# Performance work log

Hardware: AMD Instinct MI355X
Metric: run time of the kernel (lower is better)

Reference implementation:

```python
import jax, jax.numpy as jnp
import numpy as np

BOHR = 0.52917721067  # Angstrom per Bohr (au.BOHR)
A_MUTUAL = 0.39       # damping_param_mutual
N_NODES = 200_000
N_EDGES = 6_400_000


def setup_inputs() -> dict:
    key = jax.random.key(0)
    k1, k2, k3, k4, k5, k6 = jax.random.split(key, 6)
    edge_src = jax.random.randint(k1, (N_EDGES,), 0, N_NODES)
    edge_dst = jax.random.randint(k2, (N_EDGES,), 0, N_NODES)
    # displacement vectors (Angstrom); distances consistent with vec
    vec = jax.random.normal(k3, (N_EDGES, 3), dtype=jnp.float32) * 2.0
    distances = jnp.linalg.norm(vec, axis=-1) + 1e-3
    # positive polarisabilities (Angstrom^3)
    polarisability = jax.random.uniform(k4, (N_NODES,), dtype=jnp.float32) * 2.0 + 0.5
    mu = jax.random.normal(k5, (N_NODES, 3), dtype=jnp.float32) * 0.1
    species = jax.random.randint(k6, (N_NODES,), 0, 10)
    return {
        'species': species,
        'edge_src': edge_src,
        'edge_dst': edge_dst,
        'distances': distances,
        'vec': vec,
        'polarisability': polarisability,
        'mu': mu,
    }


def reference(species, edge_src, edge_dst, distances, vec, polarisability, mu):
    n_nodes = polarisability.shape[0]
    rij = distances / BOHR                 # [E]
    vec_ij = vec / BOHR                    # [E,3]
    pol = polarisability / BOHR**3         # [N]
    alpha_ij = pol[edge_dst] * pol[edge_src]   # [E]
    uij = rij / alpha_ij ** (1.0 / 6.0)
    au3 = A_MUTUAL * uij**3
    e = jnp.exp(-au3)
    lam3 = 1.0 - e                         # Thole lambda_3
    lam5 = 1.0 - (1.0 + au3) * e           # Thole lambda_5
    # Thole-damped dipole interaction matvec: T_ij mu_j
    mu_dst = mu[edge_dst]                  # [E,3] gather
    inv_r3 = 1.0 / rij**3
    inv_r5 = 1.0 / rij**5
    dot = jnp.sum(vec_ij * mu_dst, axis=-1)   # [E]
    contrib = (lam3 * inv_r3)[:, None] * mu_dst \
        - (3.0 * lam5 * inv_r5 * dot)[:, None] * vec_ij  # [E,3]
    field = jax.ops.segment_sum(contrib, edge_src, num_segments=n_nodes)  # [N,3]
    # diagonal 1/alpha term of the polarisation matrix
    return mu / pol[:, None] + field
```

## Files before the change

kernel.cpp:

```cpp
#include <hip/hip_runtime.h>
#include <math.h>


#define INV_BOHR   1.8897261254578281f
#define INV_BOHR3  (INV_BOHR*INV_BOHR*INV_BOHR)
#define A_MUTUAL   0.39f
#define NB         256
#define EPB        4096
#define SCT        512
#define GAT        1024
#define MAX_NPB    1024
#define GC_STRIDE  16

typedef float f32x4 __attribute__((ext_vector_type(4)));

__global__ void pol_node_kernel(const float* __restrict__ pol_ang,
                                const float* __restrict__ mu,
                                float* __restrict__ out,
                                float* __restrict__ q, int n_nodes) {
    int i = blockIdx.x * blockDim.x + threadIdx.x;
    if (i >= n_nodes) return;
    float pol = pol_ang[i] * INV_BOHR3;
    float ip  = 1.0f / pol;
    out[3*i + 0] = mu[3*i + 0] * ip;
    out[3*i + 1] = mu[3*i + 1] * ip;
    out[3*i + 2] = mu[3*i + 2] * ip;
    q[i] = powf(pol, -1.0f / 6.0f);
}

__device__ __forceinline__ void thole_contrib(
        float rij, float vx, float vy, float vz,
        float qs, float qd, float mx, float my, float mz,
        float& cx, float& cy, float& cz) {
    float u   = rij * qs * qd;
    float au3 = A_MUTUAL * u * u * u;
    float em1  = expm1f(-au3);
    float lam3 = -em1;
    float lam5 = -(em1 + au3 * (em1 + 1.0f));
    float inv_r  = 1.0f / rij;
    float inv_r2 = inv_r * inv_r;
    float inv_r3 = inv_r2 * inv_r;
    float inv_r5 = inv_r3 * inv_r2;
    float dot = vx*mx + vy*my + vz*mz;
    float c3  = lam3 * inv_r3;
    float c5  = 3.0f * lam5 * inv_r5 * dot;
    cx = c3*mx - c5*vx;
    cy = c3*my - c5*vy;
    cz = c3*mz - c5*vz;
}

__global__ __launch_bounds__(SCT, 4)
void pol_scatter(const int*   __restrict__ src,
                 const int*   __restrict__ dst,
                 const float* __restrict__ dist,
                 const float* __restrict__ vec,
                 const float* __restrict__ q,
                 const float* __restrict__ mu,
                 f32x4*       __restrict__ records,
                 int*         __restrict__ gcursor,
                 int e0, int e1, int npb, int cap) {
    __shared__ f32x4 stage[EPB];
    __shared__ int hist[NB];
    __shared__ int lbase[NB];
    __shared__ int scan[NB];
    __shared__ int lcur[NB];
    __shared__ int gbase[NB];

    int tid = threadIdx.x;
    int eb0 = e0 + blockIdx.x * EPB;
    int eb1 = min(eb0 + EPB, e1);
    int nrec = eb1 - eb0;
    if (nrec <= 0) return;

    if (tid < NB) hist[tid] = 0;
    __syncthreads();

    int s_reg[EPB / SCT];
    #pragma unroll
    for (int j = 0; j < EPB / SCT; ++j) {
        int e = eb0 + j * SCT + tid;
        int s = (e < eb1) ? src[e] : -1;
        s_reg[j] = s;
        if (s >= 0) atomicAdd(&hist[s / npb], 1);
    }
    __syncthreads();

    if (tid < NB) scan[tid] = hist[tid];
    __syncthreads();
    for (int off = 1; off < NB; off <<= 1) {
        int v = 0;
        if (tid < NB && tid >= off) v = scan[tid - off];
        __syncthreads();
        if (tid < NB) scan[tid] += v;
        __syncthreads();
    }
    if (tid < NB) {
        int lb = scan[tid] - hist[tid];
        lbase[tid] = lb;
        lcur[tid]  = lb;
        gbase[tid] = (hist[tid] > 0) ? atomicAdd(&gcursor[tid * GC_STRIDE], hist[tid]) : 0;
    }
    __syncthreads();

    #pragma unroll
    for (int j = 0; j < EPB / SCT; ++j) {
        int s = s_reg[j];
        if (s < 0) continue;
        int e = eb0 + j * SCT + tid;
        int   d   = __builtin_nontemporal_load(&dst[e]);
        float rij = __builtin_nontemporal_load(&dist[e]) * INV_BOHR;
        float vx  = __builtin_nontemporal_load(&vec[3*e + 0]) * INV_BOHR;
        float vy  = __builtin_nontemporal_load(&vec[3*e + 1]) * INV_BOHR;
        float vz  = __builtin_nontemporal_load(&vec[3*e + 2]) * INV_BOHR;

        float cx, cy, cz;
        thole_contrib(rij, vx, vy, vz, q[s], q[d],
                      mu[3*d + 0], mu[3*d + 1], mu[3*d + 2], cx, cy, cz);

        int b = s / npb;
        int p = atomicAdd(&lcur[b], 1);
        f32x4 rec;
        rec.x = cx; rec.y = cy; rec.z = cz; rec.w = __int_as_float(s);
        stage[p] = rec;
    }
    __syncthreads();

    for (int k = tid; k < nrec; k += SCT) {
        f32x4 f = stage[k];
        int s = __float_as_int(f.w);
        int b = s / npb;
        int slot = gbase[b] + (k - lbase[b]);
        if (slot < cap)
            records[(size_t)b * cap + slot] = f;
    }
}

__global__ __launch_bounds__(GAT, 4)
void pol_gather(const f32x4* __restrict__ records,
                const int*   __restrict__ gcursor,
                float*       __restrict__ out,
                int cap, int npb, int n_nodes) {
    __shared__ float acc[3 * MAX_NPB];
    int j   = blockIdx.x;
    int tid = threadIdx.x;
    int n0  = j * npb;
    int nn  = min(npb, n_nodes - n0);
    if (nn <= 0) return;

    for (int k = tid; k < 3 * nn; k += GAT) acc[k] = 0.0f;
    __syncthreads();

    int cnt = min(gcursor[j * GC_STRIDE], cap);
    const f32x4* rec = records + (size_t)j * cap;

    int i = tid;
    for (; i + 3 * GAT < cnt; i += 4 * GAT) {
        f32x4 r0 = __builtin_nontemporal_load(&rec[i]);
        f32x4 r1 = __builtin_nontemporal_load(&rec[i + GAT]);
        f32x4 r2 = __builtin_nontemporal_load(&rec[i + 2 * GAT]);
        f32x4 r3 = __builtin_nontemporal_load(&rec[i + 3 * GAT]);
        int l0 = __float_as_int(r0.w) - n0;
        int l1 = __float_as_int(r1.w) - n0;
        int l2 = __float_as_int(r2.w) - n0;
        int l3 = __float_as_int(r3.w) - n0;
        atomicAdd(&acc[3*l0 + 0], r0.x); atomicAdd(&acc[3*l0 + 1], r0.y); atomicAdd(&acc[3*l0 + 2], r0.z);
        atomicAdd(&acc[3*l1 + 0], r1.x); atomicAdd(&acc[3*l1 + 1], r1.y); atomicAdd(&acc[3*l1 + 2], r1.z);
        atomicAdd(&acc[3*l2 + 0], r2.x); atomicAdd(&acc[3*l2 + 1], r2.y); atomicAdd(&acc[3*l2 + 2], r2.z);
        atomicAdd(&acc[3*l3 + 0], r3.x); atomicAdd(&acc[3*l3 + 1], r3.y); atomicAdd(&acc[3*l3 + 2], r3.z);
    }
    for (; i < cnt; i += GAT) {
        f32x4 r = __builtin_nontemporal_load(&rec[i]);
        int l = __float_as_int(r.w) - n0;
        atomicAdd(&acc[3*l + 0], r.x);
        atomicAdd(&acc[3*l + 1], r.y);
        atomicAdd(&acc[3*l + 2], r.z);
    }
    __syncthreads();

    float* o = out + (size_t)3 * n0;
    for (int k = tid; k < 3 * nn; k += GAT) o[k] += acc[k];
}

__global__ void pol_edge_kernel(const int*   __restrict__ src,
                                const int*   __restrict__ dst,
                                const float* __restrict__ dist,
                                const float* __restrict__ vec,
                                const float* __restrict__ q,
                                const float* __restrict__ mu,
                                float* __restrict__ out, int n_edges) {
    int e = blockIdx.x * blockDim.x + threadIdx.x;
    if (e >= n_edges) return;
    int s = src[e], d = dst[e];
    float rij = dist[e] * INV_BOHR;
    float cx, cy, cz;
    thole_contrib(rij, vec[3*e+0]*INV_BOHR, vec[3*e+1]*INV_BOHR, vec[3*e+2]*INV_BOHR,
                  q[s], q[d], mu[3*d+0], mu[3*d+1], mu[3*d+2], cx, cy, cz);
    atomicAdd(&out[3*s + 0], cx);
    atomicAdd(&out[3*s + 1], cy);
    atomicAdd(&out[3*s + 2], cz);
}

extern "C" void kernel_launch(void* const* d_in, const int* in_sizes, int n_in,
                              void* d_out, int out_size, void* d_ws, size_t ws_size,
                              hipStream_t stream) {
    const int*   edge_src = (const int*)d_in[1];
    const int*   edge_dst = (const int*)d_in[2];
    const float* dist     = (const float*)d_in[3];
    const float* vec      = (const float*)d_in[4];
    const float* pol      = (const float*)d_in[5];
    const float* mu       = (const float*)d_in[6];

    float* out   = (float*)d_out;
    int n_nodes  = in_sizes[5];
    int n_edges  = in_sizes[1];
    int npb      = (n_nodes + NB - 1) / NB;

    size_t gc_bytes = (size_t)NB * GC_STRIDE * sizeof(int);
    size_t reserve  = gc_bytes + (size_t)n_nodes * sizeof(float) + 4096;
    int    nch = -1;
    long long cap = 0;
    size_t rec_bytes = 0;
    for (int c = 1; c <= 16; c *= 2) {
        long long chunk = ((long long)n_edges + c - 1) / c;
        long long m     = (chunk + NB - 1) / NB;
        long long cp    = m + 8 * (long long)(sqrt((double)m) + 1.0) + 64;
        size_t rb = (size_t)NB * (size_t)cp * sizeof(f32x4);
        if (rb + reserve <= ws_size) { nch = c; cap = cp; rec_bytes = rb; break; }
    }

    if (nch > 0 && npb <= MAX_NPB) {
        f32x4* records = (f32x4*)d_ws;
        int*   gcursor = (int*)((char*)d_ws + rec_bytes);
        float* q       = (float*)((char*)d_ws + rec_bytes + gc_bytes);

        pol_node_kernel<<<(n_nodes + 255) / 256, 256, 0, stream>>>(pol, mu, out, q, n_nodes);

        long long chunk = ((long long)n_edges + nch - 1) / nch;
        for (int r = 0; r < nch; ++r) {
            int e0 = (int)(r * chunk);
            int e1 = (int)min((long long)n_edges, e0 + chunk);
            if (e0 >= e1) break;
            (void)hipMemsetAsync(gcursor, 0, gc_bytes, stream);
            int nblk = (e1 - e0 + EPB - 1) / EPB;
            pol_scatter<<<nblk, SCT, 0, stream>>>(edge_src, edge_dst, dist, vec, q, mu,
                                                  records, gcursor, e0, e1, npb, (int)cap);
            pol_gather<<<NB, GAT, 0, stream>>>(records, gcursor, out, (int)cap, npb, n_nodes);
        }
    } else {
        float* q = (float*)d_ws;
        pol_node_kernel<<<(n_nodes + 255) / 256, 256, 0, stream>>>(pol, mu, out, q, n_nodes);
        pol_edge_kernel<<<(n_edges + 255) / 256, 256, 0, stream>>>(edge_src, edge_dst, dist, vec,
                                                                   q, mu, out, n_edges);
    }
}
```

Measured before the change: 426.5 us.

## Pack q and mu per node, use magic-number division, halve edges per block

The node kernel now writes a packed float4 holding (mu, q) per node, so the scatter kernel fetches the destination's q and mu with one 16-byte gather instead of four scattered loads. Integer division by npb is replaced with a multiply-shift magic number. EPB is halved and launch bounds raised to 8 to increase occupancy, src loads become nontemporal, and the gather loop is unrolled to 8 outstanding loads. The packed array is four times larger than the old q array, and the smaller blocks mean more blocks and more global cursor atomics.

Result: faster. 403.8 us (-5.3%).

```diff
diff --git a/kernel.cpp b/kernel.cpp
--- a/kernel.cpp
+++ b/kernel.cpp
@@ -6,26 +6,33 @@
 #define INV_BOHR3  (INV_BOHR*INV_BOHR*INV_BOHR)
 #define A_MUTUAL   0.39f
 #define NB         256
-#define EPB        4096
+#define EPB        2048
 #define SCT        512
 #define GAT        1024
 #define MAX_NPB    1024
 #define GC_STRIDE  16
+#define MSHIFT     40
 
 typedef float f32x4 __attribute__((ext_vector_type(4)));
+
+__device__ __forceinline__ int bdiv(int s, unsigned magic) {
+    return (int)(((unsigned long long)(unsigned)s * magic) >> MSHIFT);
+}
 
 __global__ void pol_node_kernel(const float* __restrict__ pol_ang,
                                 const float* __restrict__ mu,
                                 float* __restrict__ out,
-                                float* __restrict__ q, int n_nodes) {
+                                f32x4* __restrict__ qmu, int n_nodes) {
     int i = blockIdx.x * blockDim.x + threadIdx.x;
     if (i >= n_nodes) return;
     float pol = pol_ang[i] * INV_BOHR3;
     float ip  = 1.0f / pol;
-    out[3*i + 0] = mu[3*i + 0] * ip;
-    out[3*i + 1] = mu[3*i + 1] * ip;
-    out[3*i + 2] = mu[3*i + 2] * ip;
-    q[i] = powf(pol, -1.0f / 6.0f);
+    float mx = mu[3*i + 0], my = mu[3*i + 1], mz = mu[3*i + 2];
+    out[3*i + 0] = mx * ip;
+    out[3*i + 1] = my * ip;
+    out[3*i + 2] = mz * ip;
+    f32x4 t; t.x = mx; t.y = my; t.z = mz; t.w = powf(pol, -1.0f / 6.0f);
+    qmu[i] = t;
 }
 
 __device__ __forceinline__ void thole_contrib(
@@ -49,16 +56,15 @@
     cz = c3*mz - c5*vz;
 }
 
-__global__ __launch_bounds__(SCT, 4)
+__global__ __launch_bounds__(SCT, 8)
 void pol_scatter(const int*   __restrict__ src,
                  const int*   __restrict__ dst,
                  const float* __restrict__ dist,
                  const float* __restrict__ vec,
-                 const float* __restrict__ q,
-                 const float* __restrict__ mu,
+                 const f32x4* __restrict__ qmu,
                  f32x4*       __restrict__ records,
                  int*         __restrict__ gcursor,
-                 int e0, int e1, int npb, int cap) {
+                 int e0, int e1, int npb, int cap, unsigned magic) {
     __shared__ f32x4 stage[EPB];
     __shared__ int hist[NB];
     __shared__ int lbase[NB];
@@ -79,9 +85,9 @@
     #pragma unroll
     for (int j = 0; j < EPB / SCT; ++j) {
         int e = eb0 + j * SCT + tid;
-        int s = (e < eb1) ? src[e] : -1;
+        int s = (e < eb1) ? __builtin_nontemporal_load(&src[e]) : -1;
         s_reg[j] = s;
-        if (s >= 0) atomicAdd(&hist[s / npb], 1);
+        if (s >= 0) atomicAdd(&hist[bdiv(s, magic)], 1);
     }
     __syncthreads();
 
@@ -113,11 +119,13 @@
         float vy  = __builtin_nontemporal_load(&vec[3*e + 1]) * INV_BOHR;
         float vz  = __builtin_nontemporal_load(&vec[3*e + 2]) * INV_BOHR;
 
+        f32x4 md = qmu[d];
+        float qs = qmu[s].w;
+
         float cx, cy, cz;
-        thole_contrib(rij, vx, vy, vz, q[s], q[d],
-                      mu[3*d + 0], mu[3*d + 1], mu[3*d + 2], cx, cy, cz);
-
-        int b = s / npb;
+        thole_contrib(rij, vx, vy, vz, qs, md.w, md.x, md.y, md.z, cx, cy, cz);
+
+        int b = bdiv(s, magic);
         int p = atomicAdd(&lcur[b], 1);
         f32x4 rec;
         rec.x = cx; rec.y = cy; rec.z = cz; rec.w = __int_as_float(s);
@@ -128,7 +136,7 @@
     for (int k = tid; k < nrec; k += SCT) {
         f32x4 f = stage[k];
         int s = __float_as_int(f.w);
-        int b = s / npb;
+        int b = bdiv(s, magic);
         int slot = gbase[b] + (k - lbase[b]);
         if (slot < cap)
             records[(size_t)b * cap + slot] = f;
@@ -154,19 +162,17 @@
     const f32x4* rec = records + (size_t)j * cap;
 
     int i = tid;
-    for (; i + 3 * GAT < cnt; i += 4 * GAT) {
-        f32x4 r0 = __builtin_nontemporal_load(&rec[i]);
-        f32x4 r1 = __builtin_nontemporal_load(&rec[i + GAT]);
-        f32x4 r2 = __builtin_nontemporal_load(&rec[i + 2 * GAT]);
-        f32x4 r3 = __builtin_nontemporal_load(&rec[i + 3 * GAT]);
-        int l0 = __float_as_int(r0.w) - n0;
-        int l1 = __float_as_int(r1.w) - n0;
-        int l2 = __float_as_int(r2.w) - n0;
-        int l3 = __float_as_int(r3.w) - n0;
-        atomicAdd(&acc[3*l0 + 0], r0.x); atomicAdd(&acc[3*l0 + 1], r0.y); atomicAdd(&acc[3*l0 + 2], r0.z);
-        atomicAdd(&acc[3*l1 + 0], r1.x); atomicAdd(&acc[3*l1 + 1], r1.y); atomicAdd(&acc[3*l1 + 2], r1.z);
-        atomicAdd(&acc[3*l2 + 0], r2.x); atomicAdd(&acc[3*l2 + 1], r2.y); atomicAdd(&acc[3*l2 + 2], r2.z);
-        atomicAdd(&acc[3*l3 + 0], r3.x); atomicAdd(&acc[3*l3 + 1], r3.y); atomicAdd(&acc[3*l3 + 2], r3.z);
+    for (; i + 7 * GAT < cnt; i += 8 * GAT) {
+        f32x4 r[8];
+        #pragma unroll
+        for (int u = 0; u < 8; ++u) r[u] = __builtin_nontemporal_load(&rec[i + u * GAT]);
+        #pragma unroll
+        for (int u = 0; u < 8; ++u) {
+            int l = __float_as_int(r[u].w) - n0;
+            atomicAdd(&acc[3*l + 0], r[u].x);
+            atomicAdd(&acc[3*l + 1], r[u].y);
+            atomicAdd(&acc[3*l + 2], r[u].z);
+        }
     }
     for (; i < cnt; i += GAT) {
         f32x4 r = __builtin_nontemporal_load(&rec[i]);
@@ -179,6 +185,20 @@
 
     float* o = out + (size_t)3 * n0;
     for (int k = tid; k < 3 * nn; k += GAT) o[k] += acc[k];
+}
+
+__global__ void pol_fb_node(const float* __restrict__ pol_ang,
+                            const float* __restrict__ mu,
+                            float* __restrict__ out,
+                            float* __restrict__ q, int n_nodes) {
+    int i = blockIdx.x * blockDim.x + threadIdx.x;
+    if (i >= n_nodes) return;
+    float pol = pol_ang[i] * INV_BOHR3;
+    float ip  = 1.0f / pol;
+    out[3*i + 0] = mu[3*i + 0] * ip;
+    out[3*i + 1] = mu[3*i + 1] * ip;
+    out[3*i + 2] = mu[3*i + 2] * ip;
+    q[i] = powf(pol, -1.0f / 6.0f);
 }
 
 __global__ void pol_edge_kernel(const int*   __restrict__ src,
@@ -214,9 +234,11 @@
     int n_nodes  = in_sizes[5];
     int n_edges  = in_sizes[1];
     int npb      = (n_nodes + NB - 1) / NB;
-
-    size_t gc_bytes = (size_t)NB * GC_STRIDE * sizeof(int);
-    size_t reserve  = gc_bytes + (size_t)n_nodes * sizeof(float) + 4096;
+    unsigned magic = (unsigned)((1ULL << MSHIFT) / (unsigned)npb + 1ULL);
+
+    size_t gc_bytes  = (size_t)NB * GC_STRIDE * sizeof(int);
+    size_t qmu_bytes = (size_t)n_nodes * sizeof(f32x4);
+    size_t reserve   = gc_bytes + qmu_bytes + 4096;
     int    nch = -1;
     long long cap = 0;
     size_t rec_bytes = 0;
@@ -231,9 +253,9 @@
     if (nch > 0 && npb <= MAX_NPB) {
         f32x4* records = (f32x4*)d_ws;
         int*   gcursor = (int*)((char*)d_ws + rec_bytes);
-        float* q       = (float*)((char*)d_ws + rec_bytes + gc_bytes);
-
-        pol_node_kernel<<<(n_nodes + 255) / 256, 256, 0, stream>>>(pol, mu, out, q, n_nodes);
+        f32x4* qmu     = (f32x4*)((char*)d_ws + rec_bytes + gc_bytes);
+
+        pol_node_kernel<<<(n_nodes + 255) / 256, 256, 0, stream>>>(pol, mu, out, qmu, n_nodes);
 
         long long chunk = ((long long)n_edges + nch - 1) / nch;
         for (int r = 0; r < nch; ++r) {
@@ -242,13 +264,13 @@
             if (e0 >= e1) break;
             (void)hipMemsetAsync(gcursor, 0, gc_bytes, stream);
             int nblk = (e1 - e0 + EPB - 1) / EPB;
-            pol_scatter<<<nblk, SCT, 0, stream>>>(edge_src, edge_dst, dist, vec, q, mu,
-                                                  records, gcursor, e0, e1, npb, (int)cap);
+            pol_scatter<<<nblk, SCT, 0, stream>>>(edge_src, edge_dst, dist, vec, qmu,
+                                                  records, gcursor, e0, e1, npb, (int)cap, magic);
             pol_gather<<<NB, GAT, 0, stream>>>(records, gcursor, out, (int)cap, npb, n_nodes);
         }
     } else {
         float* q = (float*)d_ws;
-        pol_node_kernel<<<(n_nodes + 255) / 256, 256, 0, stream>>>(pol, mu, out, q, n_nodes);
+        pol_fb_node<<<(n_nodes + 255) / 256, 256, 0, stream>>>(pol, mu, out, q, n_nodes);
         pol_edge_kernel<<<(n_edges + 255) / 256, 256, 0, stream>>>(edge_src, edge_dst, dist, vec,
                                                                    q, mu, out, n_edges);
     }
```
